# Kernel tuning notes

Measured on AMD Instinct MI355X. Metric: run time of the kernel, lower is better.

The kernel has to match this reference:

```python
import jax, jax.numpy as jnp
import numpy as np

EPS = 1e-5
HEAD_SPLIT = 16   # MAB_new self.K: torch.split chunk size along channels (= head dim)
NUM_D = 16        # MAB_new self.d: becomes the number of heads; attn scale = 1/sqrt(d)


def _fc(x, W, b, g, be):
    # conv2d_ with 1x1 kernel acting on last dim + BatchNorm2d (training-mode
    # batch statistics over B,T,N per channel) + ReLU.  x: [B,T,N,Cin]
    y = jnp.einsum('btnc,oc->btno', x, W) + b
    mu = y.mean(axis=(0, 1, 2), keepdims=True)
    var = y.var(axis=(0, 1, 2), keepdims=True)  # biased var, as torch BN
    return jax.nn.relu(g * (y - mu) * jax.lax.rsqrt(var + EPS) + be)


def _mab(Q, Kin, pq, pk, pv, po):
    q = _fc(Q, *pq)
    k = _fc(Kin, *pk)
    v = _fc(Kin, *pv)
    B, Sq, N, D = q.shape
    Sk = k.shape[1]
    h = D // HEAD_SPLIT  # = NUM_D heads of size HEAD_SPLIT (split/cat quirk)
    qh = q.reshape(B, Sq, N, h, HEAD_SPLIT)
    kh = k.reshape(B, Sk, N, h, HEAD_SPLIT)
    vh = v.reshape(B, Sk, N, h, HEAD_SPLIT)
    scale = np.float32(1.0 / np.sqrt(NUM_D))
    attn = jnp.einsum('bqnhc,bknhc->bnhqk', qh, kh) * scale
    attn = jax.nn.softmax(attn, axis=-1)
    out = jnp.einsum('bnhqk,bknhc->bqnhc', attn, vh).reshape(B, Sq, N, D)
    return _fc(out, *po)


def _forward(X, TE, SE, I,
             m0qW, m0qb, m0qg, m0qz, m0kW, m0kb, m0kg, m0kz,
             m0vW, m0vb, m0vg, m0vz, m0oW, m0ob, m0og, m0oz,
             m1qW, m1qb, m1qg, m1qz, m1kW, m1kb, m1kg, m1kz,
             m1vW, m1vb, m1vg, m1vz, m1oW, m1ob, m1og, m1oz):
    mid = X
    Xc = jnp.concatenate([X, TE, SE], axis=-1)           # [B,T,N,3D]
    Ir = jnp.broadcast_to(I, (X.shape[0],) + I.shape[1:])  # [B,set_dim,N,3D]
    H = _mab(Ir, Xc, (m0qW, m0qb, m0qg, m0qz), (m0kW, m0kb, m0kg, m0kz),
             (m0vW, m0vb, m0vg, m0vz), (m0oW, m0ob, m0og, m0oz))
    res = _mab(Xc, H, (m1qW, m1qb, m1qg, m1qz), (m1kW, m1kb, m1kg, m1kz),
               (m1vW, m1vb, m1vg, m1vz), (m1oW, m1ob, m1og, m1oz))
    return mid + res


def setup_inputs() -> dict:
    key = jax.random.key(0)
    ks = list(jax.random.split(key, 64))
    B, T, N, D = 16, 12, 500, 256
    DD, S = 3 * D, 32
    nxt = iter(ks)

    def w(o, i):
        return jax.random.normal(next(nxt), (o, i), jnp.float32) * np.float32(1.0 / np.sqrt(i))

    inp = {
        'X': jax.random.normal(next(nxt), (B, T, N, D), jnp.float32),
        'TE': jax.random.normal(next(nxt), (B, T, N, D), jnp.float32),
        'SE': jax.random.normal(next(nxt), (B, T, N, D), jnp.float32),
        'I': jax.random.normal(next(nxt), (1, S, N, DD), jnp.float32) * np.float32(0.02),
    }
    layer_shapes = {'m0': [('q', D, DD), ('k', D, DD), ('v', D, DD), ('o', DD, D)],
                    'm1': [('q', D, DD), ('k', D, DD), ('v', D, DD), ('o', D, D)]}
    for pre in ('m0', 'm1'):
        for name, o, i in layer_shapes[pre]:
            inp[pre + name + 'W'] = w(o, i)
            inp[pre + name + 'b'] = jnp.zeros((o,), jnp.float32)
            inp[pre + name + 'g'] = jax.random.uniform(next(nxt), (o,), jnp.float32, 0.5, 1.5)
            inp[pre + name + 'z'] = jax.random.normal(next(nxt), (o,), jnp.float32) * np.float32(0.1)
    inp['mask'] = jnp.ones((1,), jnp.bool_)  # unused in original forward
    return inp


def reference(X, TE, SE, I,
              m0qW, m0qb, m0qg, m0qz, m0kW, m0kb, m0kg, m0kz,
              m0vW, m0vb, m0vg, m0vz, m0oW, m0ob, m0og, m0oz,
              m1qW, m1qb, m1qg, m1qz, m1kW, m1kb, m1kg, m1kz,
              m1vW, m1vb, m1vg, m1vz, m1oW, m1ob, m1og, m1oz, mask):
    return _forward(X, TE, SE, I,
                    m0qW, m0qb, m0qg, m0qz, m0kW, m0kb, m0kg, m0kz,
                    m0vW, m0vb, m0vg, m0vz, m0oW, m0ob, m0og, m0oz,
                    m1qW, m1qb, m1qg, m1qz, m1kW, m1kb, m1kg, m1kz,
                    m1vW, m1vb, m1vg, m1vz, m1oW, m1ob, m1og, m1oz)
```

## Files before the change

### kernel.cpp

```cpp
#include <hip/hip_runtime.h>
#include <stdint.h>

typedef __bf16 bf16_t;
typedef bf16_t bf16x8 __attribute__((ext_vector_type(8)));
typedef float f32x4 __attribute__((ext_vector_type(4)));

__device__ __forceinline__ float bf2f(unsigned short u) {
  union { unsigned int i; float f; } x; x.i = ((unsigned int)u) << 16; return x.f;
}
__device__ __forceinline__ unsigned short f2bf(float f) {
  union { float f; unsigned int i; } x; x.f = f;
  unsigned int r = x.i + 0x7FFFu + ((x.i >> 16) & 1u);
  return (unsigned short)(r >> 16);
}
__device__ __forceinline__ unsigned pack2(float a, float b) {
  return (unsigned)f2bf(a) | ((unsigned)f2bf(b) << 16);
}

__global__ void cat2(const float* __restrict__ a, const float* __restrict__ b,
                     float* __restrict__ dst) {
  int i = threadIdx.x;
  dst[i] = a[i]; dst[256 + i] = b[i];
}

__global__ __launch_bounds__(256) void wsplit(
    const float* __restrict__ in, unsigned short* __restrict__ hi,
    unsigned short* __restrict__ lo, int n) {
  int i = (blockIdx.x * 256 + threadIdx.x) * 8;
  if (i >= n) return;
  float4 a = *(const float4*)(in + i);
  float4 b = *(const float4*)(in + i + 4);
  float f[8] = {a.x, a.y, a.z, a.w, b.x, b.y, b.z, b.w};
  unsigned short sh[8], sl[8];
#pragma unroll
  for (int j = 0; j < 8; ++j) {
    sh[j] = f2bf(f[j]);
    sl[j] = f2bf(f[j] - bf2f(sh[j]));
  }
  *(uint4*)(hi + i) = *(uint4*)sh;
  *(uint4*)(lo + i) = *(uint4*)sl;
}

struct f8 { float4 a, b; };

__device__ __forceinline__ f8 ld_c8(const float* __restrict__ X,
                                    const float* __restrict__ TE,
                                    const float* __restrict__ SE,
                                    size_t row, int cc) {
  const float* src = (cc < 256) ? X : ((cc < 512) ? TE : SE);
  const float* p = src + row * 256 + (cc & 255);
  f8 r; r.a = *(const float4*)p; r.b = *(const float4*)(p + 4);
  return r;
}
__device__ __forceinline__ uint4 pack_hi(const float4 a, const float4 b) {
  return make_uint4(pack2(a.x, a.y), pack2(a.z, a.w), pack2(b.x, b.y), pack2(b.z, b.w));
}

template<int AMODE, int SMODE, int PART, int PREC, int K>
__global__ __launch_bounds__(512) void gemm5(
    const void* __restrict__ Ap, const float* __restrict__ AX,
    const float* __restrict__ ATE, const float* __restrict__ ASE,
    const unsigned short* __restrict__ Wh, const unsigned short* __restrict__ Wl,
    const float* __restrict__ bias, const float2* __restrict__ ssO,
    unsigned short* __restrict__ Cb, unsigned short* __restrict__ Cb2,
    float* __restrict__ psum, float* __restrict__ psq,
    int Cout, int cstr, int pOff, int nx) {
  constexpr int ASH = 64 * K;
  constexpr int TOT = ASH + (SMODE != 0 ? 64 * 136 : 8);
  __shared__ unsigned short lds[TOT];
  unsigned short* lA = lds;
  unsigned short* lC = lds + ASH;

  const int tid = threadIdx.x;
  const int lane = tid & 63, wid = tid >> 6;
  const int l15 = lane & 15, l4 = lane >> 4;
  const int brow = blockIdx.x * 64;

  constexpr int CPR = K / 8;
#pragma unroll
  for (int i = 0; i < (64 * CPR) / 512; ++i) {
    int ch = i * 512 + tid;
    int row = ch / CPR, c8 = (ch % CPR) * 8;
    uint4 hv;
    if constexpr (AMODE == 2) {
      hv = *(const uint4*)((const unsigned short*)Ap + (size_t)(brow + row) * K + c8);
    } else if constexpr (AMODE == 0) {
      const float* p = (const float*)Ap + (size_t)(brow + row) * K + c8;
      hv = pack_hi(*(const float4*)p, *(const float4*)(p + 4));
    } else {
      f8 v = ld_c8(AX, ATE, ASE, (size_t)(brow + row), c8);
      hv = pack_hi(v.a, v.b);
    }
    int dst = row * K + (c8 & ~63) + ((c8 & 63) ^ ((row & 7) << 3));
    *(uint4*)(lA + dst) = hv;
  }
  __syncthreads();

  const int axor = (l15 & 7) << 3;

  for (int cx = 0; cx < nx; ++cx) {
    const int bcol = cx * 128;
    const int colL = wid * 16 + l15;
    const int col = bcol + colL;
    const bool useLo = (PREC == 2) || (PREC == 3 && bcol >= 256);
    f32x4 acc[4] = {};

    for (int kc = 0; kc < K; kc += 256) {
      uint4 bh[8], bl[8];
      const unsigned short* wp = Wh + (size_t)col * K + kc + l4 * 8;
#pragma unroll
      for (int ks = 0; ks < 8; ++ks) bh[ks] = *(const uint4*)(wp + ks * 32);
      if (useLo) {
        const unsigned short* wq = Wl + (size_t)col * K + kc + l4 * 8;
#pragma unroll
        for (int ks = 0; ks < 8; ++ks) bl[ks] = *(const uint4*)(wq + ks * 32);
      }
#pragma unroll
      for (int kk = 0; kk < 8; ++kk) {
        const int kabs = kc + kk * 32;
        const int kt64 = kabs & ~63;
        const int cofs = ((kabs & 32) + l4 * 8) ^ axor;
        bf16x8 af[4];
#pragma unroll
        for (int m = 0; m < 4; ++m)
          af[m] = *(const bf16x8*)(lA + (m * 16 + l15) * K + kt64 + cofs);
        bf16x8 bhf = *(const bf16x8*)&bh[kk];
#pragma unroll
        for (int m = 0; m < 4; ++m)
          acc[m] = __builtin_amdgcn_mfma_f32_16x16x32_bf16(af[m], bhf, acc[m], 0, 0, 0);
        if (useLo) {
          bf16x8 blf = *(const bf16x8*)&bl[kk];
#pragma unroll
          for (int m = 0; m < 4; ++m)
            acc[m] = __builtin_amdgcn_mfma_f32_16x16x32_bf16(af[m], blf, acc[m], 0, 0, 0);
        }
      }
    }

    float cs = 0.f, cq = 0.f;
    float bv = bias[col];
    float2 s2 = make_float2(1.f, 0.f);
    if constexpr (SMODE == 2) s2 = ssO[col];
    if constexpr (SMODE != 0) __syncthreads();
#pragma unroll
    for (int m = 0; m < 4; ++m) {
#pragma unroll
      for (int r = 0; r < 4; ++r) {
        float v = acc[m][r] + bv;
        if constexpr (PART) { cs += v; cq += v * v; }
        if constexpr (SMODE == 2) v = fmaxf(v * s2.x + s2.y, 0.f);
        if constexpr (SMODE != 0) lC[(m * 16 + l4 * 4 + r) * 136 + colL] = f2bf(v);
      }
    }
    if constexpr (SMODE != 0) {
      __syncthreads();
      const int rw = tid >> 4, c16 = (tid & 15) * 8;
#pragma unroll
      for (int it = 0; it < 2; ++it) {
        int rr = it * 32 + rw;
        uint4 val = *(const uint4*)(lC + rr * 136 + c16);
        if constexpr (SMODE == 5) {
          unsigned short* dst = (bcol < 256) ? Cb : Cb2;
          *(uint4*)(dst + (size_t)(brow + rr) * 256 + (bcol & 255) + c16) = val;
        } else {
          *(uint4*)(Cb + (size_t)(brow + rr) * cstr + bcol + c16) = val;
        }
      }
    }
    if constexpr (PART) {
      cs += __shfl_xor(cs, 16); cs += __shfl_xor(cs, 32);
      cq += __shfl_xor(cq, 16); cq += __shfl_xor(cq, 32);
      if (l4 == 0) {
        size_t pidx = (size_t)(pOff + blockIdx.x) * Cout + col;
        psum[pidx] = cs;
        psq[pidx]  = cq;
      }
    }
  }
}

__global__ __launch_bounds__(256) void colstats(
    const unsigned short* __restrict__ A, float* __restrict__ psum,
    float* __restrict__ psq) {
  const int tid = threadIdx.x;
  const int r8 = tid >> 5, co = tid & 31;
  float s[8] = {0,0,0,0,0,0,0,0}, q[8] = {0,0,0,0,0,0,0,0};
  size_t base = (size_t)blockIdx.x * 2048;
  for (int it = 0; it < 256; ++it) {
    size_t row = base + it * 8 + r8;
    uint4 v = *(const uint4*)(A + row * 256 + co * 8);
    const unsigned short* pv = (const unsigned short*)&v;
#pragma unroll
    for (int j = 0; j < 8; ++j) {
      float f = bf2f(pv[j]);
      s[j] += f; q[j] += f * f;
    }
  }
  __shared__ float ls[8][32][8], lq[8][32][8];
#pragma unroll
  for (int j = 0; j < 8; ++j) { ls[r8][co][j] = s[j]; lq[r8][co][j] = q[j]; }
  __syncthreads();
  int co2 = tid >> 3, j2 = tid & 7;
  float S = 0.f, Q = 0.f;
#pragma unroll
  for (int r = 0; r < 8; ++r) { S += ls[r][co2][j2]; Q += lq[r][co2][j2]; }
  psum[(size_t)blockIdx.x * 256 + co2 * 8 + j2] = S;
  psq [(size_t)blockIdx.x * 256 + co2 * 8 + j2] = Q;
}

__global__ __launch_bounds__(512) void bn_part(
    const float* __restrict__ psum, const float* __restrict__ psq,
    float* __restrict__ pp, int gridM, int Cout) {
  const int lane = threadIdx.x & 63, wv = threadIdx.x >> 6;
  const int c = blockIdx.y * 64 + lane;
  float s = 0.f, q = 0.f;
  for (int r = blockIdx.x + 64 * wv; r < gridM; r += 512) {
    s += psum[(size_t)r * Cout + c];
    q += psq[(size_t)r * Cout + c];
  }
  __shared__ float rs[8][64], rq[8][64];
  rs[wv][lane] = s; rq[wv][lane] = q;
  __syncthreads();
  if (threadIdx.x < 64) {
    float S = 0.f, Q = 0.f;
#pragma unroll
    for (int w2 = 0; w2 < 8; ++w2) { S += rs[w2][threadIdx.x]; Q += rq[w2][threadIdx.x]; }
    pp[(size_t)blockIdx.x * Cout + blockIdx.y * 64 + threadIdx.x] = S;
    pp[(size_t)(64 + blockIdx.x) * Cout + blockIdx.y * 64 + threadIdx.x] = Q;
  }
}
__global__ __launch_bounds__(64) void bn_fin(
    const float* __restrict__ pp, const float* __restrict__ g,
    const float* __restrict__ be, float2* __restrict__ ss, int Cout, float invR) {
  int c = blockIdx.x * 64 + threadIdx.x;
  float S = 0.f, Q = 0.f;
  for (int r = 0; r < 64; ++r) {
    S += pp[(size_t)r * Cout + c];
    Q += pp[(size_t)(64 + r) * Cout + c];
  }
  float mu = S * invR, var = Q * invR - mu * mu;
  float sc = g[c] * rsqrtf(var + 1e-5f);
  ss[c] = make_float2(sc, be[c] - mu * sc);
}
__global__ __launch_bounds__(64) void bn_fin2(
    const float* __restrict__ pp, const float* __restrict__ gA,
    const float* __restrict__ zA, const float* __restrict__ gB,
    const float* __restrict__ zB, float2* __restrict__ ssC, float invR) {
  int c = blockIdx.x * 64 + threadIdx.x;
  float S = 0.f, Q = 0.f;
  for (int r = 0; r < 64; ++r) {
    S += pp[(size_t)r * 512 + c];
    Q += pp[(size_t)(64 + r) * 512 + c];
  }
  float mu = S * invR, var = Q * invR - mu * mu;
  const float* g = (c < 256) ? gA : gB;
  const float* z = (c < 256) ? zA : zB;
  int ci = c & 255;
  float sc = g[ci] * rsqrtf(var + 1e-5f);
  ssC[c] = make_float2(sc, z[ci] - mu * sc);
}

template<int NK, int NQ>
__global__ void attn_sm(const unsigned short* __restrict__ qy,
                        const unsigned short* __restrict__ ky,
                        const unsigned short* __restrict__ vy,
                        const float2* __restrict__ ssq, const float2* __restrict__ ssk,
                        const float2* __restrict__ ssv, unsigned short* __restrict__ out,
                        size_t qStride, size_t kvStride, size_t oStride, int RS) {
  __shared__ float kl[NK][16][17];
  __shared__ float vl[NK][16][17];
  const int n = blockIdx.x, b = blockIdx.y;
  const int tid = threadIdx.x;
  const unsigned short* kyb = ky + (size_t)b * kvStride;
  const unsigned short* vyb = vy + (size_t)b * kvStride;
  for (int ch = tid; ch < NK * 32; ch += NQ * 16) {
    int t = ch >> 5, c8 = (ch & 31) * 8;
    size_t src = ((size_t)t * 500 + n) * RS + c8;
    uint4 kv = *(const uint4*)(kyb + src);
    uint4 vv = *(const uint4*)(vyb + src);
    const unsigned short* kp = (const unsigned short*)&kv;
    const unsigned short* vp = (const unsigned short*)&vv;
#pragma unroll
    for (int j = 0; j < 8; ++j) {
      int c = c8 + j;
      float2 sk = ssk[c], sv = ssv[c];
      kl[t][c >> 4][c & 15] = fmaxf(bf2f(kp[j]) * sk.x + sk.y, 0.f);
      vl[t][c >> 4][c & 15] = fmaxf(bf2f(vp[j]) * sv.x + sv.y, 0.f);
    }
  }
  __syncthreads();
  const int s = tid >> 4, h = tid & 15;
  unsigned short qraw[16];
  size_t qb = (size_t)b * qStride + ((size_t)s * 500 + n) * 256 + h * 16;
  *(uint4*)qraw = *(const uint4*)(qy + qb);
  *(uint4*)(qraw + 8) = *(const uint4*)(qy + qb + 8);
  float qv[16];
#pragma unroll
  for (int c = 0; c < 16; ++c) {
    float2 sq = ssq[h * 16 + c];
    qv[c] = fmaxf(bf2f(qraw[c]) * sq.x + sq.y, 0.f);
  }
  float lg[NK], mx = -1e30f;
#pragma unroll
  for (int t = 0; t < NK; ++t) {
    float d = 0.f;
#pragma unroll
    for (int c = 0; c < 16; ++c) d += qv[c] * kl[t][h][c];
    lg[t] = d * 0.25f;
    mx = fmaxf(mx, lg[t]);
  }
  float sum = 0.f;
#pragma unroll
  for (int t = 0; t < NK; ++t) { lg[t] = __expf(lg[t] - mx); sum += lg[t]; }
  float inv = 1.f / sum;
  float o[16];
#pragma unroll
  for (int c = 0; c < 16; ++c) o[c] = 0.f;
#pragma unroll
  for (int t = 0; t < NK; ++t) {
    float p = lg[t] * inv;
#pragma unroll
    for (int c = 0; c < 16; ++c) o[c] += p * vl[t][h][c];
  }
  size_t ob = (size_t)b * oStride + ((size_t)s * 500 + n) * 256 + h * 16;
  uint4 w0;
  w0.x = pack2(o[0], o[1]); w0.y = pack2(o[2], o[3]);
  w0.z = pack2(o[4], o[5]); w0.w = pack2(o[6], o[7]);
  *(uint4*)(out + ob) = w0;
  w0.x = pack2(o[8], o[9]); w0.y = pack2(o[10], o[11]);
  w0.z = pack2(o[12], o[13]); w0.w = pack2(o[14], o[15]);
  *(uint4*)(out + ob + 8) = w0;
}

__global__ __launch_bounds__(256) void bn_relu_addx(
    const unsigned short* __restrict__ y, const float2* __restrict__ ss,
    const float* __restrict__ X, float* __restrict__ out) {
  int r = blockIdx.x * 8 + (threadIdx.x >> 5);
  int c8 = (threadIdx.x & 31) * 8;
  size_t idx = (size_t)r * 256 + c8;
  uint4 yv4 = *(const uint4*)(y + idx);
  const unsigned short* yv = (const unsigned short*)&yv4;
  float4 x0 = *(const float4*)(X + idx);
  float4 x1 = *(const float4*)(X + idx + 4);
  float ov[8];
#pragma unroll
  for (int j = 0; j < 8; ++j) {
    float2 sc = ss[c8 + j];
    ov[j] = fmaxf(bf2f(yv[j]) * sc.x + sc.y, 0.f);
  }
  *(float4*)(out + idx)     = make_float4(x0.x + ov[0], x0.y + ov[1], x0.z + ov[2], x0.w + ov[3]);
  *(float4*)(out + idx + 4) = make_float4(x1.x + ov[4], x1.y + ov[5], x1.z + ov[6], x1.w + ov[7]);
}

extern "C" void kernel_launch(void* const* d_in, const int* in_sizes, int n_in,
                              void* d_out, int out_size, void* d_ws, size_t ws_size,
                              hipStream_t stream) {
  (void)in_sizes; (void)n_in; (void)out_size; (void)ws_size;
  const float* X  = (const float*)d_in[0];
  const float* TE = (const float*)d_in[1];
  const float* SE = (const float*)d_in[2];
  const float* I  = (const float*)d_in[3];
  const float *Wf[8], *Bf[8], *Gf[8], *Zf[8];
  for (int l = 0; l < 8; ++l) {
    Wf[l] = (const float*)d_in[4 + l * 4 + 0];
    Bf[l] = (const float*)d_in[4 + l * 4 + 1];
    Gf[l] = (const float*)d_in[4 + l * 4 + 2];
    Zf[l] = (const float*)d_in[4 + l * 4 + 3];
  }

  char* w = (char*)d_ws;
  size_t off = 0;
  auto alloc = [&](size_t bytes) -> void* {
    void* p = w + off;
    off += (bytes + 255) & ~(size_t)255;
    return p;
  };

  float* psum0 = (float*)alloc((size_t)4000 * 768 * 4);
  float* psq0  = (float*)alloc((size_t)4000 * 768 * 4);
  float* psumK = (float*)alloc((size_t)125 * 256 * 4);
  float* psqK  = (float*)alloc((size_t)125 * 256 * 4);
  float* pp    = (float*)alloc((size_t)128 * 768 * 4);
  float2* ss   = (float2*)alloc((size_t)(8 * 768 + 512) * sizeof(float2));
  float2* ssC  = ss + 8 * 768;
  unsigned short *W0h, *W0l, *W3h, *W3l, *W4h, *W4l, *W7h, *W7l;
  unsigned short *KV0h, *KV0l, *KV1h, *KV1l;
  W0h = (unsigned short*)alloc(196608 * 2); W0l = (unsigned short*)alloc(196608 * 2);
  W3h = (unsigned short*)alloc(196608 * 2); W3l = (unsigned short*)alloc(196608 * 2);
  W4h = (unsigned short*)alloc(196608 * 2); W4l = (unsigned short*)alloc(196608 * 2);
  W7h = (unsigned short*)alloc(65536 * 2);  W7l = (unsigned short*)alloc(65536 * 2);
  KV0h = (unsigned short*)alloc(393216 * 2); KV0l = (unsigned short*)alloc(393216 * 2);
  KV1h = (unsigned short*)alloc(393216 * 2); KV1l = (unsigned short*)alloc(393216 * 2);
  float* b12 = (float*)alloc(512 * 4);
  float* b56 = (float*)alloc(512 * 4);
  char* R = (char*)alloc(131072000);
  unsigned short* q0  = (unsigned short*)R;
  unsigned short* kv0 = (unsigned short*)(R + 8192000);
  unsigned short* k1  = (unsigned short*)R;
  unsigned short* o0b = (unsigned short*)alloc(131072000);
  unsigned short* v1  = o0b;
  unsigned short* y7  = o0b;
  unsigned short* Hc  = (unsigned short*)alloc((size_t)32000 * 768 * 2);

  unsigned short* q1 = (unsigned short*)d_out;
  unsigned short* o1 = (unsigned short*)d_out + 24576000;

  cat2<<<dim3(1), 256, 0, stream>>>(Bf[1], Bf[2], b12);
  cat2<<<dim3(1), 256, 0, stream>>>(Bf[5], Bf[6], b56);
  wsplit<<<dim3(96), 256, 0, stream>>>(Wf[0], W0h, W0l, 196608);
  wsplit<<<dim3(96), 256, 0, stream>>>(Wf[3], W3h, W3l, 196608);
  wsplit<<<dim3(96), 256, 0, stream>>>(Wf[4], W4h, W4l, 196608);
  wsplit<<<dim3(32), 256, 0, stream>>>(Wf[7], W7h, W7l, 65536);
  wsplit<<<dim3(96), 256, 0, stream>>>(Wf[1], KV0h, KV0l, 196608);
  wsplit<<<dim3(96), 256, 0, stream>>>(Wf[2], KV0h + 196608, KV0l + 196608, 196608);
  wsplit<<<dim3(96), 256, 0, stream>>>(Wf[5], KV1h, KV1l, 196608);
  wsplit<<<dim3(96), 256, 0, stream>>>(Wf[6], KV1h + 196608, KV1l + 196608, 196608);

  auto bn1 = [&](float* ps, float* pq, const float* g, const float* z, float2* dst,
                 int gridM, int Cout, float invR) {
    bn_part<<<dim3(64, Cout / 64), 512, 0, stream>>>(ps, pq, pp, gridM, Cout);
    bn_fin<<<dim3(Cout / 64), 64, 0, stream>>>(pp, g, z, dst, Cout, invR);
  };

  gemm5<0, 1, 1, 2, 768><<<dim3(250), 512, 0, stream>>>(
      I, nullptr, nullptr, nullptr, W0h, W0l, Bf[0], nullptr,
      q0, nullptr, psum0, psq0, 256, 256, 0, 2);
  bn1(psum0, psq0, Gf[0], Zf[0], ss + 0 * 768, 250, 256, 1.f / 16000.f);
  gemm5<1, 1, 1, 2, 768><<<dim3(1500), 512, 0, stream>>>(
      nullptr, X, TE, SE, KV0h, KV0l, b12, nullptr,
      kv0, nullptr, psum0, psq0, 512, 512, 0, 4);
  bn_part<<<dim3(64, 8), 512, 0, stream>>>(psum0, psq0, pp, 1500, 512);
  bn_fin2<<<dim3(8), 64, 0, stream>>>(pp, Gf[1], Zf[1], Gf[2], Zf[2], ssC, 1.f / 96000.f);
  gemm5<1, 1, 1, 2, 768><<<dim3(1500), 512, 0, stream>>>(
      nullptr, X, TE, SE, W4h, W4l, Bf[4], nullptr,
      q1, nullptr, psum0, psq0, 256, 256, 0, 2);
  bn1(psum0, psq0, Gf[4], Zf[4], ss + 4 * 768, 1500, 256, 1.f / 96000.f);

  attn_sm<12, 32><<<dim3(500, 16), 512, 0, stream>>>(
      q0, kv0, kv0 + 256, ss + 0 * 768, ssC, ssC + 256, o0b,
      0, (size_t)6000 * 512, (size_t)16000 * 256, 512);

  gemm5<2, 0, 1, 1, 256><<<dim3(4000), 512, 0, stream>>>(
      o0b, nullptr, nullptr, nullptr, W3h, W3l, Bf[3], nullptr,
      nullptr, nullptr, psum0, psq0, 768, 768, 0, 6);
  bn1(psum0, psq0, Gf[3], Zf[3], ss + 3 * 768, 4000, 768, 1.f / 256000.f);

  for (int cb = 0; cb < 8; ++cb) {
    const size_t oCh = (size_t)cb * 32000 * 256;
    gemm5<2, 2, 0, 2, 256><<<dim3(500), 512, 0, stream>>>(
        o0b + oCh, nullptr, nullptr, nullptr, W3h, W3l, Bf[3], ss + 3 * 768,
        Hc, nullptr, nullptr, nullptr, 768, 768, 0, 6);
    gemm5<2, 5, 0, 3, 768><<<dim3(500), 512, 0, stream>>>(
        Hc, nullptr, nullptr, nullptr, KV1h, KV1l, b56, nullptr,
        k1 + oCh, v1 + oCh, nullptr, nullptr, 512, 256, 0, 4);
  }

  colstats<<<dim3(125), 256, 0, stream>>>(k1, psumK, psqK);
  bn1(psumK, psqK, Gf[5], Zf[5], ss + 5 * 768, 125, 256, 1.f / 256000.f);
  colstats<<<dim3(125), 256, 0, stream>>>(v1, psumK, psqK);
  bn1(psumK, psqK, Gf[6], Zf[6], ss + 6 * 768, 125, 256, 1.f / 256000.f);

  attn_sm<32, 12><<<dim3(500, 16), 192, 0, stream>>>(
      q1, k1, v1, ss + 4 * 768, ss + 5 * 768, ss + 6 * 768, o1,
      (size_t)6000 * 256, (size_t)16000 * 256, (size_t)6000 * 256, 256);

  gemm5<2, 1, 1, 2, 256><<<dim3(1500), 512, 0, stream>>>(
      o1, nullptr, nullptr, nullptr, W7h, W7l, Bf[7], nullptr,
      y7, nullptr, psum0, psq0, 256, 256, 0, 2);
  bn1(psum0, psq0, Gf[7], Zf[7], ss + 7 * 768, 1500, 256, 1.f / 96000.f);
  bn_relu_addx<<<dim3(12000), 256, 0, stream>>>(y7, ss + 7 * 768, X, (float*)d_out);
}
```

Measured before the change: 2.560 ms.

## Fuse q1 projection into K/V GEMM and double-buffer weight fragments

The separate m1 query projection GEMM over the concatenated input is merged with the m0 key/value GEMM into one 768-column GEMM, so the A tile (X/TE/SE concatenated and converted to bf16) is loaded and converted once instead of twice. A new store mode routes columns to kv0 and q1, and the BN statistics kernels now take a stride and column offset so they can read the combined partial sums. The GEMM inner loop also now prefetches the next 128-wide chunk of weight fragments into a double buffer, including across column tiles, to hide global load latency. This costs more registers and could lower occupancy.

```diff
diff --git a/kernel.cpp b/kernel.cpp
--- a/kernel.cpp
+++ b/kernel.cpp
@@ -17,10 +17,10 @@
   return (unsigned)f2bf(a) | ((unsigned)f2bf(b) << 16);
 }
 
-__global__ void cat2(const float* __restrict__ a, const float* __restrict__ b,
-                     float* __restrict__ dst) {
+__global__ void cat3(const float* __restrict__ a, const float* __restrict__ b,
+                     const float* __restrict__ c, float* __restrict__ dst) {
   int i = threadIdx.x;
-  dst[i] = a[i]; dst[256 + i] = b[i];
+  dst[i] = a[i]; dst[256 + i] = b[i]; dst[512 + i] = c[i];
 }
 
 __global__ __launch_bounds__(256) void wsplit(
@@ -57,7 +57,7 @@
 }
 
 template<int AMODE, int SMODE, int PART, int PREC, int K>
-__global__ __launch_bounds__(512) void gemm5(
+__global__ __launch_bounds__(512) void gemm6(
     const void* __restrict__ Ap, const float* __restrict__ AX,
     const float* __restrict__ ATE, const float* __restrict__ ASE,
     const unsigned short* __restrict__ Wh, const unsigned short* __restrict__ Wl,
@@ -67,6 +67,7 @@
     int Cout, int cstr, int pOff, int nx) {
   constexpr int ASH = 64 * K;
   constexpr int TOT = ASH + (SMODE != 0 ? 64 * 136 : 8);
+  constexpr int NC = K / 128;
   __shared__ unsigned short lds[TOT];
   unsigned short* lA = lds;
   unsigned short* lC = lds + ASH;
@@ -97,45 +98,57 @@
   __syncthreads();
 
   const int axor = (l15 & 7) << 3;
+  const int colL = wid * 16 + l15;
+
+  const unsigned short* wtH = Wh + (size_t)colL * K + l4 * 8;
+  const unsigned short* wtL = (PREC >= 2) ? (Wl + (size_t)colL * K + l4 * 8) : nullptr;
+
+  uint4 bh[2][4], bl[2][4];
+  auto ldB4 = [&](uint4* d, const unsigned short* p) {
+#pragma unroll
+    for (int ks = 0; ks < 4; ++ks) d[ks] = *(const uint4*)(p + ks * 32);
+  };
+  ldB4(bh[0], wtH);
+  if constexpr (PREC >= 2) ldB4(bl[0], wtL);
 
   for (int cx = 0; cx < nx; ++cx) {
     const int bcol = cx * 128;
-    const int colL = wid * 16 + l15;
     const int col = bcol + colL;
     const bool useLo = (PREC == 2) || (PREC == 3 && bcol >= 256);
     f32x4 acc[4] = {};
 
-    for (int kc = 0; kc < K; kc += 256) {
-      uint4 bh[8], bl[8];
-      const unsigned short* wp = Wh + (size_t)col * K + kc + l4 * 8;
-#pragma unroll
-      for (int ks = 0; ks < 8; ++ks) bh[ks] = *(const uint4*)(wp + ks * 32);
-      if (useLo) {
-        const unsigned short* wq = Wl + (size_t)col * K + kc + l4 * 8;
-#pragma unroll
-        for (int ks = 0; ks < 8; ++ks) bl[ks] = *(const uint4*)(wq + ks * 32);
+#pragma unroll
+    for (int c = 0; c < NC; ++c) {
+      if (c + 1 < NC) {
+        ldB4(bh[(c + 1) & 1], wtH + (c + 1) * 128);
+        if constexpr (PREC >= 2) ldB4(bl[(c + 1) & 1], wtL + (c + 1) * 128);
+      } else if (cx + 1 < nx) {
+        ldB4(bh[0], wtH + (size_t)128 * K);
+        if constexpr (PREC >= 2) ldB4(bl[0], wtL + (size_t)128 * K);
       }
 #pragma unroll
-      for (int kk = 0; kk < 8; ++kk) {
-        const int kabs = kc + kk * 32;
+      for (int kk = 0; kk < 4; ++kk) {
+        const int kabs = c * 128 + kk * 32;
         const int kt64 = kabs & ~63;
         const int cofs = ((kabs & 32) + l4 * 8) ^ axor;
         bf16x8 af[4];
 #pragma unroll
         for (int m = 0; m < 4; ++m)
           af[m] = *(const bf16x8*)(lA + (m * 16 + l15) * K + kt64 + cofs);
-        bf16x8 bhf = *(const bf16x8*)&bh[kk];
+        bf16x8 bhf = *(const bf16x8*)&bh[c & 1][kk];
 #pragma unroll
         for (int m = 0; m < 4; ++m)
           acc[m] = __builtin_amdgcn_mfma_f32_16x16x32_bf16(af[m], bhf, acc[m], 0, 0, 0);
         if (useLo) {
-          bf16x8 blf = *(const bf16x8*)&bl[kk];
+          bf16x8 blf = *(const bf16x8*)&bl[c & 1][kk];
 #pragma unroll
           for (int m = 0; m < 4; ++m)
             acc[m] = __builtin_amdgcn_mfma_f32_16x16x32_bf16(af[m], blf, acc[m], 0, 0, 0);
         }
       }
     }
+    wtH += (size_t)128 * K;
+    if constexpr (PREC >= 2) wtL += (size_t)128 * K;
 
     float cs = 0.f, cq = 0.f;
     float bv = bias[col];
@@ -162,6 +175,11 @@
         if constexpr (SMODE == 5) {
           unsigned short* dst = (bcol < 256) ? Cb : Cb2;
           *(uint4*)(dst + (size_t)(brow + rr) * 256 + (bcol & 255) + c16) = val;
+        } else if constexpr (SMODE == 6) {
+          if (bcol < 512)
+            *(uint4*)(Cb + (size_t)(brow + rr) * 512 + bcol + c16) = val;
+          else
+            *(uint4*)(Cb2 + (size_t)(brow + rr) * 256 + (bcol - 512) + c16) = val;
         } else {
           *(uint4*)(Cb + (size_t)(brow + rr) * cstr + bcol + c16) = val;
         }
@@ -231,26 +249,29 @@
 }
 __global__ __launch_bounds__(64) void bn_fin(
     const float* __restrict__ pp, const float* __restrict__ g,
-    const float* __restrict__ be, float2* __restrict__ ss, int Cout, float invR) {
+    const float* __restrict__ be, float2* __restrict__ ss,
+    int CoutT, int colOff, float invR) {
+  int c = blockIdx.x * 64 + threadIdx.x;
+  int cp = colOff + c;
+  float S = 0.f, Q = 0.f;
+  for (int r = 0; r < 64; ++r) {
+    S += pp[(size_t)r * CoutT + cp];
+    Q += pp[(size_t)(64 + r) * CoutT + cp];
+  }
+  float mu = S * invR, var = Q * invR - mu * mu;
+  float sc = g[c] * rsqrtf(var + 1e-5f);
+  ss[c] = make_float2(sc, be[c] - mu * sc);
+}
+__global__ __launch_bounds__(64) void bn_fin2(
+    const float* __restrict__ pp, const float* __restrict__ gA,
+    const float* __restrict__ zA, const float* __restrict__ gB,
+    const float* __restrict__ zB, float2* __restrict__ ssC,
+    int CoutT, float invR) {
   int c = blockIdx.x * 64 + threadIdx.x;
   float S = 0.f, Q = 0.f;
   for (int r = 0; r < 64; ++r) {
-    S += pp[(size_t)r * Cout + c];
-    Q += pp[(size_t)(64 + r) * Cout + c];
-  }
-  float mu = S * invR, var = Q * invR - mu * mu;
-  float sc = g[c] * rsqrtf(var + 1e-5f);
-  ss[c] = make_float2(sc, be[c] - mu * sc);
-}
-__global__ __launch_bounds__(64) void bn_fin2(
-    const float* __restrict__ pp, const float* __restrict__ gA,
-    const float* __restrict__ zA, const float* __restrict__ gB,
-    const float* __restrict__ zB, float2* __restrict__ ssC, float invR) {
-  int c = blockIdx.x * 64 + threadIdx.x;
-  float S = 0.f, Q = 0.f;
-  for (int r = 0; r < 64; ++r) {
-    S += pp[(size_t)r * 512 + c];
-    Q += pp[(size_t)(64 + r) * 512 + c];
+    S += pp[(size_t)r * CoutT + c];
+    Q += pp[(size_t)(64 + r) * CoutT + c];
   }
   float mu = S * invR, var = Q * invR - mu * mu;
   const float* g = (c < 256) ? gA : gB;
@@ -383,16 +404,15 @@
   float* pp    = (float*)alloc((size_t)128 * 768 * 4);
   float2* ss   = (float2*)alloc((size_t)(8 * 768 + 512) * sizeof(float2));
   float2* ssC  = ss + 8 * 768;
-  unsigned short *W0h, *W0l, *W3h, *W3l, *W4h, *W4l, *W7h, *W7l;
-  unsigned short *KV0h, *KV0l, *KV1h, *KV1l;
+  unsigned short *W0h, *W0l, *W3h, *W3l, *W7h, *W7l;
+  unsigned short *KVQh, *KVQl, *KV1h, *KV1l;
   W0h = (unsigned short*)alloc(196608 * 2); W0l = (unsigned short*)alloc(196608 * 2);
   W3h = (unsigned short*)alloc(196608 * 2); W3l = (unsigned short*)alloc(196608 * 2);
-  W4h = (unsigned short*)alloc(196608 * 2); W4l = (unsigned short*)alloc(196608 * 2);
   W7h = (unsigned short*)alloc(65536 * 2);  W7l = (unsigned short*)alloc(65536 * 2);
-  KV0h = (unsigned short*)alloc(393216 * 2); KV0l = (unsigned short*)alloc(393216 * 2);
+  KVQh = (unsigned short*)alloc(589824 * 2); KVQl = (unsigned short*)alloc(589824 * 2);
   KV1h = (unsigned short*)alloc(393216 * 2); KV1l = (unsigned short*)alloc(393216 * 2);
-  float* b12 = (float*)alloc(512 * 4);
-  float* b56 = (float*)alloc(512 * 4);
+  float* b124 = (float*)alloc(768 * 4);
+  float* b56  = (float*)alloc(512 * 4);
   char* R = (char*)alloc(131072000);
   unsigned short* q0  = (unsigned short*)R;
   unsigned short* kv0 = (unsigned short*)(R + 8192000);
@@ -405,52 +425,49 @@
   unsigned short* q1 = (unsigned short*)d_out;
   unsigned short* o1 = (unsigned short*)d_out + 24576000;
 
-  cat2<<<dim3(1), 256, 0, stream>>>(Bf[1], Bf[2], b12);
-  cat2<<<dim3(1), 256, 0, stream>>>(Bf[5], Bf[6], b56);
+  cat3<<<dim3(1), 256, 0, stream>>>(Bf[1], Bf[2], Bf[4], b124);
+  cat3<<<dim3(1), 256, 0, stream>>>(Bf[5], Bf[6], Bf[6], b56);
   wsplit<<<dim3(96), 256, 0, stream>>>(Wf[0], W0h, W0l, 196608);
   wsplit<<<dim3(96), 256, 0, stream>>>(Wf[3], W3h, W3l, 196608);
-  wsplit<<<dim3(96), 256, 0, stream>>>(Wf[4], W4h, W4l, 196608);
   wsplit<<<dim3(32), 256, 0, stream>>>(Wf[7], W7h, W7l, 65536);
-  wsplit<<<dim3(96), 256, 0, stream>>>(Wf[1], KV0h, KV0l, 196608);
-  wsplit<<<dim3(96), 256, 0, stream>>>(Wf[2], KV0h + 196608, KV0l + 196608, 196608);
+  wsplit<<<dim3(96), 256, 0, stream>>>(Wf[1], KVQh, KVQl, 196608);
+  wsplit<<<dim3(96), 256, 0, stream>>>(Wf[2], KVQh + 196608, KVQl + 196608, 196608);
+  wsplit<<<dim3(96), 256, 0, stream>>>(Wf[4], KVQh + 393216, KVQl + 393216, 196608);
   wsplit<<<dim3(96), 256, 0, stream>>>(Wf[5], KV1h, KV1l, 196608);
   wsplit<<<dim3(96), 256, 0, stream>>>(Wf[6], KV1h + 196608, KV1l + 196608, 196608);
 
   auto bn1 = [&](float* ps, float* pq, const float* g, const float* z, float2* dst,
                  int gridM, int Cout, float invR) {
     bn_part<<<dim3(64, Cout / 64), 512, 0, stream>>>(ps, pq, pp, gridM, Cout);
-    bn_fin<<<dim3(Cout / 64), 64, 0, stream>>>(pp, g, z, dst, Cout, invR);
+    bn_fin<<<dim3(Cout / 64), 64, 0, stream>>>(pp, g, z, dst, Cout, 0, invR);
   };
 
-  gemm5<0, 1, 1, 2, 768><<<dim3(250), 512, 0, stream>>>(
+  gemm6<0, 1, 1, 2, 768><<<dim3(250), 512, 0, stream>>>(
       I, nullptr, nullptr, nullptr, W0h, W0l, Bf[0], nullptr,
       q0, nullptr, psum0, psq0, 256, 256, 0, 2);
   bn1(psum0, psq0, Gf[0], Zf[0], ss + 0 * 768, 250, 256, 1.f / 16000.f);
-  gemm5<1, 1, 1, 2, 768><<<dim3(1500), 512, 0, stream>>>(
-      nullptr, X, TE, SE, KV0h, KV0l, b12, nullptr,
-      kv0, nullptr, psum0, psq0, 512, 512, 0, 4);
-  bn_part<<<dim3(64, 8), 512, 0, stream>>>(psum0, psq0, pp, 1500, 512);
-  bn_fin2<<<dim3(8), 64, 0, stream>>>(pp, Gf[1], Zf[1], Gf[2], Zf[2], ssC, 1.f / 96000.f);
-  gemm5<1, 1, 1, 2, 768><<<dim3(1500), 512, 0, stream>>>(
-      nullptr, X, TE, SE, W4h, W4l, Bf[4], nullptr,
-      q1, nullptr, psum0, psq0, 256, 256, 0, 2);
-  bn1(psum0, psq0, Gf[4], Zf[4], ss + 4 * 768, 1500, 256, 1.f / 96000.f);
+  gemm6<1, 6, 1, 2, 768><<<dim3(1500), 512, 0, stream>>>(
+      nullptr, X, TE, SE, KVQh, KVQl, b124, nullptr,
+      kv0, q1, psum0, psq0, 768, 0, 0, 6);
+  bn_part<<<dim3(64, 12), 512, 0, stream>>>(psum0, psq0, pp, 1500, 768);
+  bn_fin2<<<dim3(8), 64, 0, stream>>>(pp, Gf[1], Zf[1], Gf[2], Zf[2], ssC, 768, 1.f / 96000.f);
+  bn_fin<<<dim3(4), 64, 0, stream>>>(pp, Gf[4], Zf[4], ss + 4 * 768, 768, 512, 1.f / 96000.f);
 
   attn_sm<12, 32><<<dim3(500, 16), 512, 0, stream>>>(
       q0, kv0, kv0 + 256, ss + 0 * 768, ssC, ssC + 256, o0b,
       0, (size_t)6000 * 512, (size_t)16000 * 256, 512);
 
-  gemm5<2, 0, 1, 1, 256><<<dim3(4000), 512, 0, stream>>>(
+  gemm6<2, 0, 1, 1, 256><<<dim3(4000), 512, 0, stream>>>(
       o0b, nullptr, nullptr, nullptr, W3h, W3l, Bf[3], nullptr,
       nullptr, nullptr, psum0, psq0, 768, 768, 0, 6);
   bn1(psum0, psq0, Gf[3], Zf[3], ss + 3 * 768, 4000, 768, 1.f / 256000.f);
 
   for (int cb = 0; cb < 8; ++cb) {
     const size_t oCh = (size_t)cb * 32000 * 256;
-    gemm5<2, 2, 0, 2, 256><<<dim3(500), 512, 0, stream>>>(
+    gemm6<2, 2, 0, 2, 256><<<dim3(500), 512, 0, stream>>>(
         o0b + oCh, nullptr, nullptr, nullptr, W3h, W3l, Bf[3], ss + 3 * 768,
         Hc, nullptr, nullptr, nullptr, 768, 768, 0, 6);
-    gemm5<2, 5, 0, 3, 768><<<dim3(500), 512, 0, stream>>>(
+    gemm6<2, 5, 0, 3, 768><<<dim3(500), 512, 0, stream>>>(
         Hc, nullptr, nullptr, nullptr, KV1h, KV1l, b56, nullptr,
         k1 + oCh, v1 + oCh, nullptr, nullptr, 512, 256, 0, 4);
   }
@@ -464,7 +481,7 @@
       q1, k1, v1, ss + 4 * 768, ss + 5 * 768, ss + 6 * 768, o1,
       (size_t)6000 * 256, (size_t)16000 * 256, (size_t)6000 * 256, 256);
 
-  gemm5<2, 1, 1, 2, 256><<<dim3(1500), 512, 0, stream>>>(
+  gemm6<2, 1, 1, 2, 256><<<dim3(1500), 512, 0, stream>>>(
       o1, nullptr, nullptr, nullptr, W7h, W7l, Bf[7], nullptr,
       y7, nullptr, psum0, psq0, 256, 256, 0, 2);
   bn1(psum0, psq0, Gf[7], Zf[7], ss + 7 * 768, 1500, 256, 1.f / 96000.f);
```

After: 2.683 ms. 1.05x slower.
